# Optimization experiments

Hardware: AMD Instinct MI355X
Metric: run time of the kernel (lower is better)

## Reference

```python
import jax, jax.numpy as jnp
import numpy as np

# Search geometry (matches init_kwargs)
WS, WT, PS, K, STRIDE0 = 9, 1, 7, 10, 4
SEARCH_INPUT = "noisy"
ALPHA = 0.5
CRIT = "l2"


def _extract_patches(vid, ti, hi, wi):
    """vid: [T,H,W,C]; ti/hi/wi int32 with shape [...] (patch top-left corners).
    Returns [..., PS*PS*C] with clamped (edge-replicated) boundary handling."""
    T, H, W, C = vid.shape
    dy = jnp.arange(PS)
    dx = jnp.arange(PS)
    hh = jnp.clip(hi[..., None, None] + dy[:, None], 0, H - 1)  # [...,PS,1]
    ww = jnp.clip(wi[..., None, None] + dx[None, :], 0, W - 1)  # [...,1,PS]
    p = vid[ti[..., None, None], hh, ww]  # [...,PS,PS,C]
    return p.reshape(p.shape[:-3] + (PS * PS * C,))


def _nls(vid, fflow, bflow):
    """NonLocalSearch: vid [T,H,W,C], flows [T,H,W,2] (channel 0 = x/w, 1 = y/h).
    Returns (topk_dists [nq,K], inds = (ti,hi,wi,tk,hk,wk))."""
    T, H, W, C = vid.shape
    nH, nW = H // STRIDE0, W // STRIDE0
    ti, hi, wi = jnp.meshgrid(jnp.arange(T), jnp.arange(nH) * STRIDE0,
                              jnp.arange(nW) * STRIDE0, indexing="ij")
    ti, hi, wi = ti.reshape(-1), hi.reshape(-1), wi.reshape(-1)  # [nq]
    q = _extract_patches(vid, ti, hi, wi)  # [nq, PS*PS*C]

    ff = fflow[ti, hi, wi]  # [nq,2] flow to frame t+1
    bf = bflow[ti, hi, wi]  # [nq,2] flow to frame t-1
    zero = jnp.zeros_like(ff)
    flow_dt = jnp.stack([bf, zero, ff], axis=1)  # [nq, 2*WT+1, 2] for dt=-1,0,+1
    dts = jnp.arange(-WT, WT + 1)
    tj = jnp.clip(ti[:, None] + dts[None, :], 0, T - 1)  # [nq, 2*WT+1]
    bh = jnp.clip(hi[:, None] + jnp.round(flow_dt[..., 1]).astype(jnp.int32), 0, H - 1)
    bw = jnp.clip(wi[:, None] + jnp.round(flow_dt[..., 0]).astype(jnp.int32), 0, W - 1)

    # Candidate schedule: (dt_index, oy, ox) for all (2*WT+1)*WS*WS candidates.
    r = WS // 2
    oy, ox = np.meshgrid(np.arange(-r, r + 1), np.arange(-r, r + 1), indexing="ij")
    nt = 2 * WT + 1
    specs = np.stack([np.repeat(np.arange(nt), WS * WS),
                      np.tile(oy.ravel(), nt),
                      np.tile(ox.ravel(), nt)], axis=1).astype(np.int32)  # [S,3]

    def step(_, spec):
        di, sy, sx = spec[0], spec[1], spec[2]
        tjc = tj[:, di]
        hj = jnp.clip(bh[:, di] + sy, 0, H - 1)
        wj = jnp.clip(bw[:, di] + sx, 0, W - 1)
        cp = _extract_patches(vid, tjc, hj, wj)  # [nq,D]
        d = jnp.sum((q - cp) ** 2, axis=-1)  # L2 patch distance, [nq]
        return None, (d, tjc, hj, wj)

    _, (dists, tjs, hjs, wjs) = jax.lax.scan(step, None, jnp.asarray(specs))
    # dists: [S, nq] -> top-K smallest per query
    negd, idx = jax.lax.top_k(-dists.T, K)  # [nq,K]
    tk = jnp.take_along_axis(tjs.T, idx, axis=1)
    hk = jnp.take_along_axis(hjs.T, idx, axis=1)
    wk = jnp.take_along_axis(wjs.T, idx, axis=1)
    return -negd, (ti, hi, wi, tk, hk, wk)


def _refine(vid, inds):
    """RefineSearch with wr=1,kr=1: recompute L2 patch distances at given inds."""
    ti, hi, wi, tk, hk, wk = inds
    q = _extract_patches(vid, ti, hi, wi)          # [nq, D]
    cp = _extract_patches(vid, tk, hk, wk)         # [nq, K, D]
    return jnp.sum((q[:, None, :] - cp) ** 2, axis=-1)  # [nq, K]


def setup_inputs() -> dict:
    key = jax.random.key(0)
    k1, k2, k3, k4 = jax.random.split(key, 4)
    B, T, C, H, W = 1, 5, 3, 384, 384
    noisy = jax.random.normal(k1, (B, T, C, H, W), dtype=jnp.float32)
    deno = jax.random.normal(k2, (B, T, C, H, W), dtype=jnp.float32)
    fflow = jax.random.normal(k3, (B, T, 2, H, W), dtype=jnp.float32)
    bflow = jax.random.normal(k4, (B, T, 2, H, W), dtype=jnp.float32)
    return {"noisy": noisy, "deno": deno, "fflow": fflow, "bflow": bflow}


def reference(noisy, deno, fflow, bflow):
    def per_video(nv, dv, ff, bf):
        nv_t = jnp.transpose(nv, (0, 2, 3, 1))  # [T,H,W,C]
        dv_t = jnp.transpose(dv, (0, 2, 3, 1))
        ff_t = jnp.transpose(ff, (0, 2, 3, 1))  # [T,H,W,2]
        bf_t = jnp.transpose(bf, (0, 2, 3, 1))
        if SEARCH_INPUT == "noisy":
            srch = nv_t
        elif SEARCH_INPUT == "deno":
            srch = dv_t
        else:  # interp
            srch = ALPHA * nv_t + (1.0 - ALPHA) * dv_t
        _, inds = _nls(srch, ff_t, bf_t)
        return _refine(nv_t, inds)  # [nq, K]

    dists = jax.vmap(per_video)(noisy, deno, fflow, bflow)  # [B, nq, K]
    if CRIT == "l1":
        return jnp.mean(jnp.sqrt(dists))
    return jnp.mean(dists)
```

## Files before the change

### kernel.cpp

```cpp
#include <hip/hip_runtime.h>

#define TT 5
#define HH 384
#define WW 384
#define CC 3
#define WSR 4
#define NH_ 96
#define NW_ 96
#define NQ_ (TT*NH_*NW_)
#define NCAND 243
#define KK 10

#define RROW 12

typedef _Float16 h2v __attribute__((ext_vector_type(2)));
union U32H2 { unsigned u; h2v h; };

static __device__ __forceinline__ unsigned pack_f16(float a, float b) {
    U32H2 u;
    u.h.x = (_Float16)a; u.h.y = (_Float16)b;
    return u.u;
}

static __device__ __forceinline__ unsigned wave_min63(unsigned x) {
    x = min(x, (unsigned)__builtin_amdgcn_update_dpp((int)x,(int)x,0x121,0xF,0xF,false));
    x = min(x, (unsigned)__builtin_amdgcn_update_dpp((int)x,(int)x,0x122,0xF,0xF,false));
    x = min(x, (unsigned)__builtin_amdgcn_update_dpp((int)x,(int)x,0x124,0xF,0xF,false));
    x = min(x, (unsigned)__builtin_amdgcn_update_dpp((int)x,(int)x,0x128,0xF,0xF,false));
    x = min(x, (unsigned)__builtin_amdgcn_update_dpp((int)x,(int)x,0x142,0xF,0xF,false));
    x = min(x, (unsigned)__builtin_amdgcn_update_dpp((int)x,(int)x,0x143,0xF,0xF,false));
    return x;
}

__global__ __launch_bounds__(64, 4) void nls_kernel(
    const float* __restrict__ vid,
    const float* __restrict__ fflow,
    const float* __restrict__ bflow,
    float* __restrict__ ws)
{
    const int bid  = blockIdx.x;
    const int q    = (bid & 7) * (NQ_/8) + (bid >> 3);
    const int lane = threadIdx.x;
    const int t    = q / (NH_*NW_);
    const int rem  = q % (NH_*NW_);
    const int hi   = (rem / NW_) * 4;
    const int wi   = (rem % NW_) * 4;

    __shared__ alignas(16) unsigned reg_lds[135*RROW];
    __shared__ alignas(16) unsigned qp_lds[84];
    __shared__ float rssd[630];

    const float ffx = fflow[((t*2+0)*HH + hi)*WW + wi];
    const float ffy = fflow[((t*2+1)*HH + hi)*WW + wi];
    const float bfx = bflow[((t*2+0)*HH + hi)*WW + wi];
    const float bfy = bflow[((t*2+1)*HH + hi)*WW + wi];

    const int tj0 = max(t-1, 0);
    const int tj2 = min(t+1, TT-1);
    const int bh0 = min(max(hi + (int)rintf(bfy), 0), HH-1);
    const int bw0 = min(max(wi + (int)rintf(bfx), 0), WW-1);
    const int bh2 = min(max(hi + (int)rintf(ffy), 0), HH-1);
    const int bw2 = min(max(wi + (int)rintf(ffx), 0), WW-1);
    const int rm0 = max(bh0-WSR,0), rm1 = max(hi-WSR,0), rm2 = max(bh2-WSR,0);
    const int cm0 = max(bw0-WSR,0), cm1 = max(wi-WSR,0), cm2 = max(bw2-WSR,0);
    const int ca0 = cm0 & ~1,       ca1 = cm1 & ~1,      ca2 = cm2 & ~1;

    for (int i = lane; i < 270; i += 64) {
        int row = i >> 1, h = i & 1;
        int di  = row / 45; int r45 = row - di*45;
        int c   = r45 / 15; int r   = r45 - c*15;
        int tjd = (di==0)?tj0:((di==1)?t  :tj2);
        int rm  = (di==0)?rm0:((di==1)?rm1:rm2);
        int ca  = (di==0)?ca0:((di==1)?ca1:ca2);
        int rr  = min(rm + r, HH-1);
        const float* vrow = vid + (size_t)((tjd*CC+c)*HH + rr)*WW;
        int c0 = ca + 8*h;
        float f0,f1,f2,f3,f4,f5,f6,f7;
        if (ca <= 368) {
            float2 p0 = *(const float2*)(vrow + c0);
            float2 p1 = *(const float2*)(vrow + c0 + 2);
            float2 p2 = *(const float2*)(vrow + c0 + 4);
            float2 p3 = *(const float2*)(vrow + c0 + 6);
            f0=p0.x; f1=p0.y; f2=p1.x; f3=p1.y; f4=p2.x; f5=p2.y; f6=p3.x; f7=p3.y;
        } else {
            f0=vrow[min(c0,  WW-1)]; f1=vrow[min(c0+1,WW-1)];
            f2=vrow[min(c0+2,WW-1)]; f3=vrow[min(c0+3,WW-1)];
            f4=vrow[min(c0+4,WW-1)]; f5=vrow[min(c0+5,WW-1)];
            f6=vrow[min(c0+6,WW-1)]; f7=vrow[min(c0+7,WW-1)];
        }
        uint4 w;
        w.x = pack_f16(f0,f1); w.y = pack_f16(f2,f3);
        w.z = pack_f16(f4,f5); w.w = pack_f16(f6,f7);
        *(uint4*)&reg_lds[row*RROW + 4*h] = w;
    }
    for (int i = lane; i < 84; i += 64) {
        int c  = i / 28;
        int rr = i - c*28;
        int dy = rr >> 2;
        int k  = rr & 3;
        int row = min(hi+dy, HH-1);
        const float* vrow = vid + (size_t)((t*CC + c)*HH + row)*WW;
        float v0 = vrow[min(wi + 2*k, WW-1)];
        float v1 = (k==3) ? 0.0f : vrow[min(wi + 2*k + 1, WW-1)];
        qp_lds[i] = pack_f16(v0, v1);
    }
    __syncthreads();

    unsigned k0 = 0xFFFFFFFFu, k1 = 0xFFFFFFFFu, k2 = 0xFFFFFFFFu, k3 = 0xFFFFFFFFu;

    for (int di = 0; di < 3; ++di) {
        if (lane < 63) {
            int roff = lane / 7, dy = lane - roff*7;
            int rr   = roff + dy;
            float rs[10];
            #pragma unroll
            for (int w = 0; w < 10; w++) rs[w] = 0.f;
            #pragma unroll
            for (int c = 0; c < 3; c++) {
                int base = ((di*3 + c)*15 + rr)*RROW;
                uint4 va0 = *(const uint4*)&reg_lds[base];
                uint4 va1 = *(const uint4*)&reg_lds[base + 4];
                uint4 vq  = *(const uint4*)&qp_lds[c*28 + dy*4];
                unsigned A[8], B[8];
                A[0]=va0.x; A[1]=va0.y; A[2]=va0.z; A[3]=va0.w;
                A[4]=va1.x; A[5]=va1.y; A[6]=va1.z; A[7]=va1.w;
                #pragma unroll
                for (int j = 0; j < 7; j++) B[j] = (A[j] >> 16) | (A[j+1] << 16);
                B[7] = A[7] >> 16;
                U32H2 q0,q1,q2,q3;
                q0.u = vq.x; q1.u = vq.y; q2.u = vq.z; q3.u = vq.w;
                #pragma unroll
                for (int w = 0; w < 10; w++) {
                    const int off = w >> 1;
                    U32H2 c0,c1,c2,c3;
                    if (w & 1) { c0.u=B[off]; c1.u=B[off+1]; c2.u=B[off+2]; c3.u=B[off+3]; }
                    else       { c0.u=A[off]; c1.u=A[off+1]; c2.u=A[off+2]; c3.u=A[off+3]; }
                    U32H2 d0,d1,d2,d3;
                    d0.h = c0.h - q0.h;
                    d1.h = c1.h - q1.h;
                    d2.h = c2.h - q2.h;
                    d3.h = c3.h - q3.h;
                    d3.u &= 0x0000FFFFu;
                    float s = rs[w];
                    s = __builtin_amdgcn_fdot2(d0.h, d0.h, s, false);
                    s = __builtin_amdgcn_fdot2(d1.h, d1.h, s, false);
                    s = __builtin_amdgcn_fdot2(d2.h, d2.h, s, false);
                    s = __builtin_amdgcn_fdot2(d3.h, d3.h, s, false);
                    rs[w] = s;
                }
            }
            int ob = lane * 10;
            #pragma unroll
            for (int w = 0; w < 10; w++) rssd[ob + w] = rs[w];
        }
        __syncthreads();

        const int bhd = (di==0)?bh0:((di==1)?hi :bh2);
        const int bwd = (di==0)?bw0:((di==1)?wi :bw2);
        const int rm  = (di==0)?rm0:((di==1)?rm1:rm2);
        const int ca  = (di==0)?ca0:((di==1)?ca1:ca2);
        #pragma unroll
        for (int j = 0; j < 4; j++) {
            int c   = j*64 + lane;
            int s81 = c - di*81;
            if (s81 >= 0 && s81 < 81) {
                int syq = s81 / 9;
                int sx  = s81 - syq*9 - WSR;
                int sy  = syq - WSR;
                int hj = min(max(bhd + sy, 0), HH-1);
                int wj = min(max(bwd + sx, 0), WW-1);
                int roff = hj - rm;
                int wof  = wj - ca;
                int ib = roff*70 + wof;
                float s = 0.f;
                #pragma unroll
                for (int dy = 0; dy < 7; dy++) s += rssd[ib + dy*10];
                unsigned key = (__float_as_uint(s) & 0xFFFFFF00u) | (unsigned)c;
                if (j==0) k0 = key;
                if (j==1) k1 = key;
                if (j==2) k2 = key;
                if (j==3) k3 = key;
            }
        }
        __syncthreads();
    }

    {
        float sumk = 0.f;
        #pragma unroll 1
        for (int k = 0; k < KK; k++) {
            unsigned loc = min(min(k0,k1), min(k2,k3));
            unsigned wm  = wave_min63(loc);
            unsigned m   = (unsigned)__builtin_amdgcn_readlane((int)wm, 63);
            sumk += __uint_as_float(m & 0xFFFFFF00u);
            int slot = (int)(m & 0xFFu);
            k0 = (slot == lane      ) ? 0xFFFFFFFFu : k0;
            k1 = (slot == lane + 64 ) ? 0xFFFFFFFFu : k1;
            k2 = (slot == lane + 128) ? 0xFFFFFFFFu : k2;
            k3 = (slot == lane + 192) ? 0xFFFFFFFFu : k3;
        }
        if (lane == 0) ws[q] = sumk;
    }
}

__global__ __launch_bounds__(256) void reduce1_kernel(
    const float* __restrict__ ws, float* __restrict__ out)
{
    float s = ws[blockIdx.x*256 + threadIdx.x];
    #pragma unroll
    for (int o = 32; o > 0; o >>= 1) s += __shfl_down(s, o, 64);
    __shared__ float sd[4];
    int w = threadIdx.x >> 6, l = threadIdx.x & 63;
    if (l == 0) sd[w] = s;
    __syncthreads();
    if (threadIdx.x == 0) {
        float tot = sd[0] + sd[1] + sd[2] + sd[3];
        atomicAdd(out, tot * (1.0f / ((float)NQ_ * (float)KK)));
    }
}

extern "C" void kernel_launch(void* const* d_in, const int* in_sizes, int n_in,
                              void* d_out, int out_size, void* d_ws, size_t ws_size,
                              hipStream_t stream) {
    const float* noisy = (const float*)d_in[0];
    const float* fflow = (const float*)d_in[2];
    const float* bflow = (const float*)d_in[3];
    float* ws  = (float*)d_ws;
    float* out = (float*)d_out;

    hipMemsetAsync(out, 0, sizeof(float), stream);
    nls_kernel<<<NQ_, 64, 0, stream>>>(noisy, fflow, bflow, ws);
    reduce1_kernel<<<NQ_/256, 256, 0, stream>>>(ws, out);
}
```

Measured before the change: 269.8 us.

## Pack four queries per block and load search rows directly from global

Each 256-thread block now processes four queries, one per wave, with per-wave LDS slices synchronized by wave-local lgkmcnt fences instead of block barriers. The staging of the search region into LDS is removed; each lane loads its reference row directly from global memory and converts it to fp16 in registers. This is meant to cut the staging pass, the block barriers, and the launch and occupancy cost of 64-thread blocks. In exchange, each lane issues redundant global loads (rows shared across lanes are re-read), which now depend on L1/L2 hits. It also relies on the wave-only fence being sufficient for LDS ordering within a wave.

New measurement: 370.2 us. 37.2% more time.

```diff
diff --git a/kernel.cpp b/kernel.cpp
--- a/kernel.cpp
+++ b/kernel.cpp
@@ -8,10 +8,9 @@
 #define NH_ 96
 #define NW_ 96
 #define NQ_ (TT*NH_*NW_)
+#define NBLK (NQ_/4)
 #define NCAND 243
 #define KK 10
-
-#define RROW 12
 
 typedef _Float16 h2v __attribute__((ext_vector_type(2)));
 union U32H2 { unsigned u; h2v h; };
@@ -20,6 +19,11 @@
     U32H2 u;
     u.h.x = (_Float16)a; u.h.y = (_Float16)b;
     return u.u;
+}
+
+static __device__ __forceinline__ void wave_fence() {
+    asm volatile("s_waitcnt lgkmcnt(0)" ::: "memory");
+    __builtin_amdgcn_sched_barrier(0);
 }
 
 static __device__ __forceinline__ unsigned wave_min63(unsigned x) {
@@ -32,23 +36,26 @@
     return x;
 }
 
-__global__ __launch_bounds__(64, 4) void nls_kernel(
+__global__ __launch_bounds__(256, 8) void nls_kernel(
     const float* __restrict__ vid,
     const float* __restrict__ fflow,
     const float* __restrict__ bflow,
     float* __restrict__ ws)
 {
     const int bid  = blockIdx.x;
-    const int q    = (bid & 7) * (NQ_/8) + (bid >> 3);
-    const int lane = threadIdx.x;
+    const int blk  = (bid & 7) * (NBLK/8) + (bid >> 3);
+    const int wid  = threadIdx.x >> 6;
+    const int lane = threadIdx.x & 63;
+    const int q    = blk*4 + wid;
     const int t    = q / (NH_*NW_);
     const int rem  = q % (NH_*NW_);
     const int hi   = (rem / NW_) * 4;
     const int wi   = (rem % NW_) * 4;
 
-    __shared__ alignas(16) unsigned reg_lds[135*RROW];
-    __shared__ alignas(16) unsigned qp_lds[84];
-    __shared__ float rssd[630];
+    __shared__ float    rssd_all[4*630];
+    __shared__ unsigned qp_all[4*84];
+    float*    rssd = rssd_all + wid*630;
+    unsigned* qp   = qp_all   + wid*84;
 
     const float ffx = fflow[((t*2+0)*HH + hi)*WW + wi];
     const float ffy = fflow[((t*2+1)*HH + hi)*WW + wi];
@@ -65,34 +72,6 @@
     const int cm0 = max(bw0-WSR,0), cm1 = max(wi-WSR,0), cm2 = max(bw2-WSR,0);
     const int ca0 = cm0 & ~1,       ca1 = cm1 & ~1,      ca2 = cm2 & ~1;
 
-    for (int i = lane; i < 270; i += 64) {
-        int row = i >> 1, h = i & 1;
-        int di  = row / 45; int r45 = row - di*45;
-        int c   = r45 / 15; int r   = r45 - c*15;
-        int tjd = (di==0)?tj0:((di==1)?t  :tj2);
-        int rm  = (di==0)?rm0:((di==1)?rm1:rm2);
-        int ca  = (di==0)?ca0:((di==1)?ca1:ca2);
-        int rr  = min(rm + r, HH-1);
-        const float* vrow = vid + (size_t)((tjd*CC+c)*HH + rr)*WW;
-        int c0 = ca + 8*h;
-        float f0,f1,f2,f3,f4,f5,f6,f7;
-        if (ca <= 368) {
-            float2 p0 = *(const float2*)(vrow + c0);
-            float2 p1 = *(const float2*)(vrow + c0 + 2);
-            float2 p2 = *(const float2*)(vrow + c0 + 4);
-            float2 p3 = *(const float2*)(vrow + c0 + 6);
-            f0=p0.x; f1=p0.y; f2=p1.x; f3=p1.y; f4=p2.x; f5=p2.y; f6=p3.x; f7=p3.y;
-        } else {
-            f0=vrow[min(c0,  WW-1)]; f1=vrow[min(c0+1,WW-1)];
-            f2=vrow[min(c0+2,WW-1)]; f3=vrow[min(c0+3,WW-1)];
-            f4=vrow[min(c0+4,WW-1)]; f5=vrow[min(c0+5,WW-1)];
-            f6=vrow[min(c0+6,WW-1)]; f7=vrow[min(c0+7,WW-1)];
-        }
-        uint4 w;
-        w.x = pack_f16(f0,f1); w.y = pack_f16(f2,f3);
-        w.z = pack_f16(f4,f5); w.w = pack_f16(f6,f7);
-        *(uint4*)&reg_lds[row*RROW + 4*h] = w;
-    }
     for (int i = lane; i < 84; i += 64) {
         int c  = i / 28;
         int rr = i - c*28;
@@ -102,31 +81,48 @@
         const float* vrow = vid + (size_t)((t*CC + c)*HH + row)*WW;
         float v0 = vrow[min(wi + 2*k, WW-1)];
         float v1 = (k==3) ? 0.0f : vrow[min(wi + 2*k + 1, WW-1)];
-        qp_lds[i] = pack_f16(v0, v1);
-    }
-    __syncthreads();
+        qp[i] = pack_f16(v0, v1);
+    }
+    wave_fence();
 
     unsigned k0 = 0xFFFFFFFFu, k1 = 0xFFFFFFFFu, k2 = 0xFFFFFFFFu, k3 = 0xFFFFFFFFu;
+    const int roff9 = lane / 7;
+    const int dy7   = lane - roff9*7;
 
     for (int di = 0; di < 3; ++di) {
+        const int tjd = (di==0)?tj0:((di==1)?t  :tj2);
+        const int rm  = (di==0)?rm0:((di==1)?rm1:rm2);
+        const int ca  = (di==0)?ca0:((di==1)?ca1:ca2);
+        const int bhd = (di==0)?bh0:((di==1)?hi :bh2);
+        const int bwd = (di==0)?bw0:((di==1)?wi :bw2);
+
         if (lane < 63) {
-            int roff = lane / 7, dy = lane - roff*7;
-            int rr   = roff + dy;
+            const int rowg = min(rm + roff9 + dy7, HH-1);
             float rs[10];
             #pragma unroll
             for (int w = 0; w < 10; w++) rs[w] = 0.f;
             #pragma unroll
             for (int c = 0; c < 3; c++) {
-                int base = ((di*3 + c)*15 + rr)*RROW;
-                uint4 va0 = *(const uint4*)&reg_lds[base];
-                uint4 va1 = *(const uint4*)&reg_lds[base + 4];
-                uint4 vq  = *(const uint4*)&qp_lds[c*28 + dy*4];
+                const float* vrow = vid + (size_t)((tjd*CC+c)*HH + rowg)*WW;
                 unsigned A[8], B[8];
-                A[0]=va0.x; A[1]=va0.y; A[2]=va0.z; A[3]=va0.w;
-                A[4]=va1.x; A[5]=va1.y; A[6]=va1.z; A[7]=va1.w;
+                if (ca <= WW-16) {
+                    #pragma unroll
+                    for (int j = 0; j < 8; j++) {
+                        float2 p = *(const float2*)(vrow + ca + 2*j);
+                        A[j] = pack_f16(p.x, p.y);
+                    }
+                } else {
+                    #pragma unroll
+                    for (int j = 0; j < 8; j++) {
+                        float v0 = vrow[min(ca+2*j,   WW-1)];
+                        float v1 = vrow[min(ca+2*j+1, WW-1)];
+                        A[j] = pack_f16(v0, v1);
+                    }
+                }
                 #pragma unroll
                 for (int j = 0; j < 7; j++) B[j] = (A[j] >> 16) | (A[j+1] << 16);
                 B[7] = A[7] >> 16;
+                uint4 vq = *(const uint4*)&qp[c*28 + dy7*4];
                 U32H2 q0,q1,q2,q3;
                 q0.u = vq.x; q1.u = vq.y; q2.u = vq.z; q3.u = vq.w;
                 #pragma unroll
@@ -149,16 +145,12 @@
                     rs[w] = s;
                 }
             }
-            int ob = lane * 10;
+            const int ob = lane * 10;
             #pragma unroll
             for (int w = 0; w < 10; w++) rssd[ob + w] = rs[w];
         }
-        __syncthreads();
-
-        const int bhd = (di==0)?bh0:((di==1)?hi :bh2);
-        const int bwd = (di==0)?bw0:((di==1)?wi :bw2);
-        const int rm  = (di==0)?rm0:((di==1)?rm1:rm2);
-        const int ca  = (di==0)?ca0:((di==1)?ca1:ca2);
+        wave_fence();
+
         #pragma unroll
         for (int j = 0; j < 4; j++) {
             int c   = j*64 + lane;
@@ -182,7 +174,7 @@
                 if (j==3) k3 = key;
             }
         }
-        __syncthreads();
+        wave_fence();
     }
 
     {
@@ -229,6 +221,6 @@
     float* out = (float*)d_out;
 
     hipMemsetAsync(out, 0, sizeof(float), stream);
-    nls_kernel<<<NQ_, 64, 0, stream>>>(noisy, fflow, bflow, ws);
+    nls_kernel<<<NBLK, 256, 0, stream>>>(noisy, fflow, bflow, ws);
     reduce1_kernel<<<NQ_/256, 256, 0, stream>>>(ws, out);
 }
```
